# Kernel tuning notes

Measured on AMD Instinct MI355X. Metric: run time of the kernel, lower is better.

Reference implementation:

```python
import jax, jax.numpy as jnp
import numpy as np

EMBED_DIM = 1024
NUM_HEADS = 16
HEAD_DIM = EMBED_DIM // NUM_HEADS
SCALE = HEAD_DIM ** -0.5


def setup_inputs() -> dict:
    key = jax.random.key(0)
    ks = jax.random.split(key, 9)
    B, S, E = 2, 2048, EMBED_DIM
    std = E ** -0.5
    return {
        "x": jax.random.normal(ks[0], (B, S, E), dtype=jnp.float32),
        "Wq": jax.random.normal(ks[1], (E, E), dtype=jnp.float32) * std,
        "bq": jax.random.normal(ks[2], (E,), dtype=jnp.float32) * 0.01,
        "Wk": jax.random.normal(ks[3], (E, E), dtype=jnp.float32) * std,
        "bk": jax.random.normal(ks[4], (E,), dtype=jnp.float32) * 0.01,
        "Wv": jax.random.normal(ks[5], (E, E), dtype=jnp.float32) * std,
        "bv": jax.random.normal(ks[6], (E,), dtype=jnp.float32) * 0.01,
        "Wo": jax.random.normal(ks[7], (E, E), dtype=jnp.float32) * std,
        "bo": jax.random.normal(ks[8], (E,), dtype=jnp.float32) * 0.01,
    }


def reference(x, Wq, bq, Wk, bk, Wv, bv, Wo, bo):
    B, S, E = x.shape
    H, D = NUM_HEADS, HEAD_DIM
    # torch Linear: y = x @ W.T + b
    q = (x @ Wq.T + bq).reshape(B, S, H, D).transpose(0, 2, 1, 3)  # [B,H,S,D]
    k = (x @ Wk.T + bk).reshape(B, S, H, D).transpose(0, 2, 1, 3)
    v = (x @ Wv.T + bv).reshape(B, S, H, D).transpose(0, 2, 1, 3)
    attn = jnp.einsum("bhqd,bhkd->bhqk", q, k) * SCALE  # [B,H,S,S]
    # NOTE: original code softmaxes over dim=1 (the heads axis) — faithful repro.
    attn = jax.nn.softmax(attn.astype(jnp.float32), axis=1).astype(q.dtype)
    out = jnp.einsum("bhqk,bhkd->bhqd", attn, v)  # [B,H,S,D]
    out = out.transpose(0, 2, 1, 3).reshape(B, S, E)
    out = out @ Wo.T + bo
    return out, attn
```

## Files before the change

### kernel.cpp

```cpp
#include <hip/hip_runtime.h>

typedef _Float16 hf2 __attribute__((ext_vector_type(2)));
typedef _Float16 hf4 __attribute__((ext_vector_type(4)));
typedef _Float16 hf8 __attribute__((ext_vector_type(8)));
typedef float    fx4 __attribute__((ext_vector_type(4)));

#define GLD16(gp, lp) __builtin_amdgcn_global_load_lds(                      \
    (const __attribute__((address_space(1))) void*)(gp),                     \
    (__attribute__((address_space(3))) void*)(lp), 16, 0, 0)

__global__ __launch_bounds__(256) void cvt_x_k(const float* __restrict__ s,
                                               _Float16* __restrict__ d) {
  size_t i = (size_t)blockIdx.x * 256 + threadIdx.x;
  float4 v = ((const float4*)s)[i];
  hf4 o = {(_Float16)v.x, (_Float16)v.y, (_Float16)v.z, (_Float16)v.w};
  *(hf4*)(d + 4 * i) = o;
}

__global__ __launch_bounds__(256) void cvt_w_k(const float* __restrict__ s0,
                                               const float* __restrict__ s1,
                                               const float* __restrict__ s2,
                                               const float* __restrict__ s3,
                                               _Float16* __restrict__ d) {
  const float* s = blockIdx.y == 0 ? s0 : blockIdx.y == 1 ? s1 : blockIdx.y == 2 ? s2 : s3;
  size_t i = (size_t)blockIdx.x * 256 + threadIdx.x;
  float4 v = ((const float4*)s)[i];
  hf4 o = {(_Float16)v.x, (_Float16)v.y, (_Float16)v.z, (_Float16)v.w};
  *(hf4*)(d + (size_t)blockIdx.y * 1048576 + 4 * i) = o;
}

__device__ __forceinline__ void gemm_tile(
    const _Float16* __restrict__ A, const _Float16* __restrict__ B,
    const float* __restrict__ bias, _Float16* __restrict__ Ch,
    float* __restrict__ Cf, int m0, int n0, int ldc, int mode)
{
  __shared__ alignas(16) _Float16 Asm[2][128 * 32];
  __shared__ alignas(16) _Float16 Bsm[2][128 * 32];
  const int tid = (int)threadIdx.x;
  const int lane = tid & 63, wv = tid >> 6;
  const int col = lane & 15, g = lane >> 4;

  fx4 acc[2][8];
#pragma unroll
  for (int i = 0; i < 2; ++i)
#pragma unroll
    for (int j = 0; j < 8; ++j) acc[i][j] = fx4{0.f, 0.f, 0.f, 0.f};

  const int cp0 = tid, cp1 = tid + 256;
  const int row0 = cp0 >> 2, row1 = cp1 >> 2;
  const int ch0 = (cp0 & 3) ^ ((row0 >> 1) & 3);
  const int ch1 = (cp1 & 3) ^ ((row1 >> 1) & 3);
  const _Float16* a0 = A + (size_t)(m0 + row0) * 1024 + ch0 * 8;
  const _Float16* a1 = A + (size_t)(m0 + row1) * 1024 + ch1 * 8;
  const _Float16* b0 = B + (size_t)(n0 + row0) * 1024 + ch0 * 8;
  const _Float16* b1 = B + (size_t)(n0 + row1) * 1024 + ch1 * 8;

  int aoff[2], boff[8];
#pragma unroll
  for (int mi = 0; mi < 2; ++mi) {
    int row = wv * 32 + mi * 16 + col;
    aoff[mi] = (row * 4 + (g ^ ((row >> 1) & 3))) * 8;
  }
#pragma unroll
  for (int nj = 0; nj < 8; ++nj) {
    int row = nj * 16 + col;
    boff[nj] = (row * 4 + (g ^ ((row >> 1) & 3))) * 8;
  }

#define STAGE_T(bufi, kt) {                          \
    GLD16(a0 + (kt) * 32, &Asm[bufi][cp0 * 8]);      \
    GLD16(a1 + (kt) * 32, &Asm[bufi][cp1 * 8]);      \
    GLD16(b0 + (kt) * 32, &Bsm[bufi][cp0 * 8]);      \
    GLD16(b1 + (kt) * 32, &Bsm[bufi][cp1 * 8]); }

  STAGE_T(0, 0);
  int buf = 0;
  for (int kt = 0; kt < 32; ++kt) {
    __syncthreads();
    if (kt + 1 < 32) STAGE_T(buf ^ 1, kt + 1);
    hf8 af[2], bf[8];
#pragma unroll
    for (int mi = 0; mi < 2; ++mi) af[mi] = *(const hf8*)&Asm[buf][aoff[mi]];
#pragma unroll
    for (int nj = 0; nj < 8; ++nj) bf[nj] = *(const hf8*)&Bsm[buf][boff[nj]];
#pragma unroll
    for (int mi = 0; mi < 2; ++mi)
#pragma unroll
      for (int nj = 0; nj < 8; ++nj)
        acc[mi][nj] = __builtin_amdgcn_mfma_f32_16x16x32_f16(af[mi], bf[nj], acc[mi][nj], 0, 0, 0);
    buf ^= 1;
  }
#undef STAGE_T

  if (mode == 2) {
#pragma unroll
    for (int nj = 0; nj < 8; ++nj) {
      float bn = bias[n0 + nj * 16 + col];
#pragma unroll
      for (int mi = 0; mi < 2; ++mi)
#pragma unroll
        for (int r = 0; r < 4; ++r)
          Cf[(size_t)(m0 + wv * 32 + mi * 16 + 4 * g + r) * ldc + n0 + nj * 16 + col] =
              acc[mi][nj][r] + bn;
    }
  } else if (mode == 0) {
#pragma unroll
    for (int nj = 0; nj < 8; ++nj) {
      float bn = bias[n0 + nj * 16 + col];
#pragma unroll
      for (int mi = 0; mi < 2; ++mi)
#pragma unroll
        for (int r = 0; r < 4; ++r)
          Ch[(size_t)(m0 + wv * 32 + mi * 16 + 4 * g + r) * ldc + n0 + nj * 16 + col] =
              (_Float16)(acc[mi][nj][r] + bn);
    }
  } else {
#pragma unroll
    for (int mi = 0; mi < 2; ++mi)
#pragma unroll
      for (int r = 0; r < 4; ++r) {
        float bm = bias[m0 + wv * 32 + mi * 16 + 4 * g + r];
#pragma unroll
        for (int nj = 0; nj < 8; ++nj)
          Ch[(size_t)(m0 + wv * 32 + mi * 16 + 4 * g + r) * ldc + n0 + nj * 16 + col] =
              (_Float16)(acc[mi][nj][r] + bm);
      }
  }
}

__global__ __launch_bounds__(256, 3) void qkv_gemm_k(
    const _Float16* __restrict__ xh, const _Float16* __restrict__ Wqh,
    const _Float16* __restrict__ Wkh, const _Float16* __restrict__ Wvh,
    const float* __restrict__ bq, const float* __restrict__ bk,
    const float* __restrict__ bv, _Float16* __restrict__ Qh,
    _Float16* __restrict__ Kh, _Float16* __restrict__ Vt)
{
  int id = (int)blockIdx.x;
  if (id < 512) {
    int t = id & 255;
    const _Float16* Bp = (id < 256) ? Wqh : Wkh;
    const float*    bp = (id < 256) ? bq : bk;
    _Float16*       Cp = (id < 256) ? Qh : Kh;
    gemm_tile(xh, Bp, bp, Cp, nullptr, (t >> 3) * 128, (t & 7) * 128, 1024, 0);
  } else {
    int t = id - 512;
    gemm_tile(Wvh, xh, bv, Vt, nullptr, (t >> 5) * 128, (t & 31) * 128, 4096, 1);
  }
}

__global__ __launch_bounds__(256, 3) void out_gemm_k(
    const _Float16* __restrict__ Oh, const _Float16* __restrict__ Woh,
    const float* __restrict__ bo, float* __restrict__ outp)
{
  int id = (int)blockIdx.x;
  gemm_tile(Oh, Woh, bo, nullptr, outp, (id >> 3) * 128, (id & 7) * 128, 1024, 2);
}

__global__ __launch_bounds__(256) void repack_v_k(const _Float16* __restrict__ Vt,
                                                  _Float16* __restrict__ V2) {
  const int tid = (int)threadIdx.x;
  const int kgi = (int)blockIdx.x;
  const int h = (int)blockIdx.y, b = (int)blockIdx.z;
  const int k0 = kgi * 128;
  __shared__ alignas(16) _Float16 Vl[64 * 128];
#pragma unroll
  for (int i = 0; i < 4; ++i) {
    int s = tid + i * 256;
    int er = s >> 4, c = s & 15;
    GLD16(Vt + (size_t)(h * 64 + er) * 4096 + b * 2048 + k0 + ((c ^ (er & 15)) * 8),
          Vl + s * 8);
  }
  __syncthreads();
  const int lane = tid & 63, dtsub = tid >> 6;
  const int col = lane & 15, g = lane >> 4;
  const int er = dtsub * 16 + col;
  _Float16* out = V2 + ((((size_t)(b * 16 + h) * 128 + (k0 >> 4)) * 4 + dtsub) * 256) + lane * 4;
#pragma unroll
  for (int ks = 0; ks < 8; ++ks) {
    int cl = 2 * ks + (g >> 1);
    int phys = cl ^ col;
    hf4 v = *(const hf4*)&Vl[er * 128 + phys * 8 + (g & 1) * 4];
    *(hf4*)(out + (size_t)ks * 1024) = v;
  }
}

__global__ __launch_bounds__(256, 4) void qk_stats_k(
    const _Float16* __restrict__ Qh, const _Float16* __restrict__ Kh,
    float* __restrict__ C0, float* __restrict__ C1)
{
  const int tid = (int)threadIdx.x;
  const int lane = tid & 63, wv = tid >> 6;
  const int col = lane & 15, g = lane >> 4;
  const int id = (int)blockIdx.x;
  const int xcd = id & 7, j = id >> 3;
  const int b = xcd >> 2, qq = xcd & 3;
  const int kx = j >> 5, qyl = j & 31;
  const int q0 = (qq * 32 + qyl) * 16;
  const int kt0 = kx * 64;

  __shared__ alignas(16) _Float16 Kt[2][4096];
  __shared__ alignas(16) _Float16 Qt[2][1024];

  const _Float16* Kbase = Kh + (size_t)(b * 2048 + kt0) * 1024;
  const _Float16* Qbase = Qh + (size_t)(b * 2048 + q0) * 1024;
  const int kr0 = tid >> 3,         kc0 = tid & 7;
  const int kr1 = (tid + 256) >> 3, kc1 = (tid + 256) & 7;
  const int qr = tid >> 3,          qc = tid & 7;

#define STG1(bufi, h) {                                                       \
    GLD16(Kbase + (size_t)kr0 * 1024 + (h) * 64 + (kc0 ^ (kr0 & 7)) * 8,      \
          &Kt[bufi][tid * 8]);                                                \
    GLD16(Kbase + (size_t)kr1 * 1024 + (h) * 64 + (kc1 ^ (kr1 & 7)) * 8,      \
          &Kt[bufi][(tid + 256) * 8]);                                        \
    if (tid < 128)                                                            \
      GLD16(Qbase + (size_t)qr * 1024 + (h) * 64 + (qc ^ (qr & 7)) * 8,       \
            &Qt[bufi][tid * 8]); }

  fx4 lg[16];
#pragma unroll
  for (int h = 0; h < 16; ++h) lg[h] = fx4{0.f, 0.f, 0.f, 0.f};

  STG1(0, 0);
  int buf = 0;
  const int krow = wv * 16 + col;
#pragma unroll
  for (int h = 0; h < 16; ++h) {
    __syncthreads();
    if (h < 15) STG1(buf ^ 1, h + 1);
    hf8 ka0 = *(const hf8*)&Kt[buf][krow * 64 + ((0 + g) ^ (krow & 7)) * 8];
    hf8 ka1 = *(const hf8*)&Kt[buf][krow * 64 + ((4 + g) ^ (krow & 7)) * 8];
    hf8 qa0 = *(const hf8*)&Qt[buf][col * 64 + ((0 + g) ^ (col & 7)) * 8];
    hf8 qa1 = *(const hf8*)&Qt[buf][col * 64 + ((4 + g) ^ (col & 7)) * 8];
    lg[h] = __builtin_amdgcn_mfma_f32_16x16x32_f16(ka0, qa0, lg[h], 0, 0, 0);
    lg[h] = __builtin_amdgcn_mfma_f32_16x16x32_f16(ka1, qa1, lg[h], 0, 0, 0);
    buf ^= 1;
  }
#undef STG1

  fx4 mx = lg[0];
#pragma unroll
  for (int h = 1; h < 16; ++h)
#pragma unroll
    for (int r = 0; r < 4; ++r) mx[r] = fmaxf(mx[r], lg[h][r]);
  fx4 sm = fx4{0.f, 0.f, 0.f, 0.f};
#pragma unroll
  for (int h = 0; h < 16; ++h)
#pragma unroll
    for (int r = 0; r < 4; ++r) sm[r] += __expf((lg[h][r] - mx[r]) * 0.125f);
  fx4 C;
#pragma unroll
  for (int r = 0; r < 4; ++r) C[r] = mx[r] * 0.125f + __logf(sm[r]);

  float* Cb = b ? C1 : C0;
  const int ktp = kx * 4 + wv;
  const int qt  = qq * 32 + qyl;
  *(fx4*)(Cb + ((size_t)ktp * 128 + qt) * 256 + lane * 4) = C;
}

__global__ __launch_bounds__(512, 4) void pv_attn_k(
    const _Float16* __restrict__ Qh, const _Float16* __restrict__ Kh,
    const _Float16* __restrict__ V2, const float* __restrict__ C0,
    const float* __restrict__ C1, float* __restrict__ attnp,
    _Float16* __restrict__ Oh)
{
  const int tid = (int)threadIdx.x;
  const int lane = tid & 63, wv = tid >> 6;
  const int col = lane & 15, g = lane >> 4;
  const int id = (int)blockIdx.x;
  const int lin = (id & 7) * 256 + (id >> 3);
  const int b = lin >> 10, qt32 = (lin >> 4) & 63, h = lin & 15;
  const int q0 = qt32 * 32;

  __shared__ alignas(16) _Float16 Kt[2][8192];
  __shared__ alignas(16) _Float16 Qt[2048];
  __shared__ alignas(16) float    sst[2][16][136];

  const _Float16* Kbh = Kh + (size_t)(b * 2048) * 1024 + h * 64;
  const float*    Cb  = b ? C1 : C0;

#define STGK2(bufi, kc) {                                                     \
    int r0_ = tid >> 3, c0_ = tid & 7;                                        \
    int r1_ = (tid + 512) >> 3, c1_ = (tid + 512) & 7;                        \
    GLD16(Kbh + (size_t)((kc) * 128 + r0_) * 1024 + (c0_ ^ (r0_ & 7)) * 8,    \
          &Kt[bufi][tid * 8]);                                                \
    GLD16(Kbh + (size_t)((kc) * 128 + r1_) * 1024 + (c1_ ^ (r1_ & 7)) * 8,    \
          &Kt[bufi][(tid + 512) * 8]); }

  if (tid < 256) {
    int qr_ = tid >> 3, qc_ = tid & 7;
    GLD16(Qh + (size_t)(b * 2048 + q0 + qr_) * 1024 + h * 64 + (qc_ ^ (qr_ & 7)) * 8,
          &Qt[tid * 8]);
  }

  fx4 acc[2][4];
#pragma unroll
  for (int t = 0; t < 2; ++t)
#pragma unroll
    for (int dt = 0; dt < 4; ++dt) acc[t][dt] = fx4{0.f, 0.f, 0.f, 0.f};

  STGK2(0, 0);
  int buf = 0;
  const int krow = wv * 16 + col;
  const int srow = 2 * wv + (lane >> 5);
  const int sks  = (lane & 31) * 4;
  float* attnbase = attnp + (size_t)((b * 16 + h) * 2048 + q0) * 2048;
  const _Float16* v2h = V2 + (size_t)(b * 16 + h) * 131072 + lane * 4;

  for (int kc = 0; kc < 16; ++kc) {
    __syncthreads();
    if (kc < 15) STGK2(buf ^ 1, kc + 1);

    hf8 ka0 = *(const hf8*)&Kt[buf][krow * 64 + ((0 + g) ^ (krow & 7)) * 8];
    hf8 ka1 = *(const hf8*)&Kt[buf][krow * 64 + ((4 + g) ^ (krow & 7)) * 8];

    const int ksg = kc * 8 + wv;
    const _Float16* v2b = v2h + (size_t)ksg * 1024;
    hf4 vb[4];
#pragma unroll
    for (int dt = 0; dt < 4; ++dt) vb[dt] = *(const hf4*)(v2b + dt * 256);

#pragma unroll
    for (int t = 0; t < 2; ++t) {
      const int qrow = t * 16 + col;
      hf8 qa0 = *(const hf8*)&Qt[qrow * 64 + ((0 + g) ^ (qrow & 7)) * 8];
      hf8 qa1 = *(const hf8*)&Qt[qrow * 64 + ((4 + g) ^ (qrow & 7)) * 8];
      fx4 lg = fx4{0.f, 0.f, 0.f, 0.f};
      lg = __builtin_amdgcn_mfma_f32_16x16x32_f16(ka0, qa0, lg, 0, 0, 0);
      lg = __builtin_amdgcn_mfma_f32_16x16x32_f16(ka1, qa1, lg, 0, 0, 0);

      fx4 cc = *(const fx4*)(Cb + ((size_t)ksg * 128 + qt32 * 2 + t) * 256 + lane * 4);
      fx4 av;
#pragma unroll
      for (int r = 0; r < 4; ++r) av[r] = __expf(lg[r] * 0.125f - cc[r]);

      hf4 pa = {(_Float16)av[0], (_Float16)av[1], (_Float16)av[2], (_Float16)av[3]};
#pragma unroll
      for (int dt = 0; dt < 4; ++dt)
        acc[t][dt] = __builtin_amdgcn_mfma_f32_16x16x16f16(pa, vb[dt], acc[t][dt], 0, 0, 0);

      *(fx4*)&sst[t][col][wv * 16 + 4 * g] = av;
    }
    __syncthreads();

#pragma unroll
    for (int t = 0; t < 2; ++t) {
      fx4 val = *(const fx4*)&sst[t][srow][sks];
      __builtin_nontemporal_store(
          val, (fx4*)(attnbase + (size_t)(t * 16 + srow) * 2048 + kc * 128 + sks));
    }
    buf ^= 1;
  }
#undef STGK2

  float* Osum = &sst[0][0][0];
  for (int w = 0; w < 8; ++w) {
    __syncthreads();
    if (wv == w) {
#pragma unroll
      for (int t = 0; t < 2; ++t)
#pragma unroll
        for (int dt = 0; dt < 4; ++dt)
#pragma unroll
          for (int r = 0; r < 4; ++r) {
            int idx = (t * 16 + 4 * g + r) * 64 + dt * 16 + col;
            Osum[idx] = (w == 0) ? acc[t][dt][r] : Osum[idx] + acc[t][dt][r];
          }
    }
  }
  __syncthreads();
  {
    int q = tid >> 4, e4 = (tid & 15) * 4;
    hf4 o = {(_Float16)Osum[q * 64 + e4],     (_Float16)Osum[q * 64 + e4 + 1],
             (_Float16)Osum[q * 64 + e4 + 2], (_Float16)Osum[q * 64 + e4 + 3]};
    *(hf4*)(Oh + (size_t)(b * 2048 + q0 + q) * 1024 + h * 64 + e4) = o;
  }
}

extern "C" void kernel_launch(void* const* d_in, const int* in_sizes, int n_in,
                              void* d_out, int out_size, void* d_ws, size_t ws_size,
                              hipStream_t stream) {
  (void)in_sizes; (void)n_in; (void)out_size; (void)ws_size;
  const float* x  = (const float*)d_in[0];
  const float* Wq = (const float*)d_in[1];
  const float* bq = (const float*)d_in[2];
  const float* Wk = (const float*)d_in[3];
  const float* bk = (const float*)d_in[4];
  const float* Wv = (const float*)d_in[5];
  const float* bv = (const float*)d_in[6];
  const float* Wo = (const float*)d_in[7];
  const float* bo = (const float*)d_in[8];

  char* ws = (char*)d_ws;
  _Float16* xh   = (_Float16*)(ws + (0ull  << 20));
  _Float16* V2   = (_Float16*)(ws + (0ull  << 20));
  _Float16* Wqh  = (_Float16*)(ws + (8ull  << 20));
  _Float16* Wkh  = (_Float16*)(ws + (10ull << 20));
  _Float16* Wvh  = (_Float16*)(ws + (12ull << 20));
  _Float16* Woh  = (_Float16*)(ws + (14ull << 20));
  _Float16* Qh   = (_Float16*)(ws + (16ull << 20));
  _Float16* Kh   = (_Float16*)(ws + (24ull << 20));
  _Float16* Vt   = (_Float16*)(ws + (32ull << 20));
  _Float16* Oh   = (_Float16*)(ws + (40ull << 20));
  float*    C1   = (float*)   (ws + (48ull << 20));

  float* outp  = (float*)d_out;
  float* C0    = outp;
  float* attnp = outp + 4194304ull;

  cvt_x_k<<<4096, 256, 0, stream>>>(x, xh);
  cvt_w_k<<<dim3(1024, 4), 256, 0, stream>>>(Wq, Wk, Wv, Wo, Wqh);
  qkv_gemm_k<<<768, 256, 0, stream>>>(xh, Wqh, Wkh, Wvh, bq, bk, bv, Qh, Kh, Vt);
  repack_v_k<<<dim3(16, 16, 2), 256, 0, stream>>>(Vt, V2);
  qk_stats_k<<<8192, 256, 0, stream>>>(Qh, Kh, C0, C1);
  pv_attn_k<<<2048, 512, 0, stream>>>(Qh, Kh, V2, C0, C1, attnp, Oh);
  out_gemm_k<<<256, 256, 0, stream>>>(Oh, Woh, bo, outp);
}
```

Measured before the change: 299.3 us.

## Stage two heads per step in QK stats; double query tile in PV attention

The QK-statistics kernel now loads K and Q tiles covering two heads (128 columns) per pipeline step with a 16-way XOR swizzle. That halves the number of barrier/prefetch iterations. The PV-attention kernel now processes 64 query rows per block instead of 32 and is launched with half as many blocks, so each staged K tile and V fragment is reused across twice as many queries. The trade-off is larger LDS use and more accumulator registers, which may lower occupancy. The Osum reduction buffer must also hold 64x64 floats, which fits within the enlarged sst array.

```diff
diff --git a/kernel.cpp b/kernel.cpp
--- a/kernel.cpp
+++ b/kernel.cpp
@@ -198,23 +198,22 @@
   const int q0 = (qq * 32 + qyl) * 16;
   const int kt0 = kx * 64;
 
-  __shared__ alignas(16) _Float16 Kt[2][4096];
-  __shared__ alignas(16) _Float16 Qt[2][1024];
+  __shared__ alignas(16) _Float16 Kt[2][8192];
+  __shared__ alignas(16) _Float16 Qt[2][2048];
 
   const _Float16* Kbase = Kh + (size_t)(b * 2048 + kt0) * 1024;
   const _Float16* Qbase = Qh + (size_t)(b * 2048 + q0) * 1024;
-  const int kr0 = tid >> 3,         kc0 = tid & 7;
-  const int kr1 = (tid + 256) >> 3, kc1 = (tid + 256) & 7;
-  const int qr = tid >> 3,          qc = tid & 7;
-
-#define STG1(bufi, h) {                                                       \
-    GLD16(Kbase + (size_t)kr0 * 1024 + (h) * 64 + (kc0 ^ (kr0 & 7)) * 8,      \
-          &Kt[bufi][tid * 8]);                                                \
-    GLD16(Kbase + (size_t)kr1 * 1024 + (h) * 64 + (kc1 ^ (kr1 & 7)) * 8,      \
-          &Kt[bufi][(tid + 256) * 8]);                                        \
-    if (tid < 128)                                                            \
-      GLD16(Qbase + (size_t)qr * 1024 + (h) * 64 + (qc ^ (qr & 7)) * 8,       \
-            &Qt[bufi][tid * 8]); }
+
+#define STG1(bufi, hp) {                                                      \
+    _Pragma("unroll")                                                         \
+    for (int i_ = 0; i_ < 4; ++i_) {                                          \
+      int s_ = tid + i_ * 256, r_ = s_ >> 4, pc_ = s_ & 15;                   \
+      GLD16(Kbase + (size_t)r_ * 1024 + (hp) * 128 + ((pc_ ^ (r_ & 15)) * 8), \
+            &Kt[bufi][s_ * 8]);                                               \
+    }                                                                         \
+    { int r_ = tid >> 4, pc_ = tid & 15;                                      \
+      GLD16(Qbase + (size_t)r_ * 1024 + (hp) * 128 + ((pc_ ^ r_) * 8),        \
+            &Qt[bufi][tid * 8]); } }
 
   fx4 lg[16];
 #pragma unroll
@@ -224,15 +223,19 @@
   int buf = 0;
   const int krow = wv * 16 + col;
 #pragma unroll
-  for (int h = 0; h < 16; ++h) {
+  for (int hp = 0; hp < 8; ++hp) {
     __syncthreads();
-    if (h < 15) STG1(buf ^ 1, h + 1);
-    hf8 ka0 = *(const hf8*)&Kt[buf][krow * 64 + ((0 + g) ^ (krow & 7)) * 8];
-    hf8 ka1 = *(const hf8*)&Kt[buf][krow * 64 + ((4 + g) ^ (krow & 7)) * 8];
-    hf8 qa0 = *(const hf8*)&Qt[buf][col * 64 + ((0 + g) ^ (col & 7)) * 8];
-    hf8 qa1 = *(const hf8*)&Qt[buf][col * 64 + ((4 + g) ^ (col & 7)) * 8];
-    lg[h] = __builtin_amdgcn_mfma_f32_16x16x32_f16(ka0, qa0, lg[h], 0, 0, 0);
-    lg[h] = __builtin_amdgcn_mfma_f32_16x16x32_f16(ka1, qa1, lg[h], 0, 0, 0);
+    if (hp < 7) STG1(buf ^ 1, hp + 1);
+#pragma unroll
+    for (int hh = 0; hh < 2; ++hh) {
+      const int h = 2 * hp + hh;
+      hf8 ka0 = *(const hf8*)&Kt[buf][krow * 128 + (((hh * 8 + 0 + g) ^ (krow & 15)) * 8)];
+      hf8 ka1 = *(const hf8*)&Kt[buf][krow * 128 + (((hh * 8 + 4 + g) ^ (krow & 15)) * 8)];
+      hf8 qa0 = *(const hf8*)&Qt[buf][col * 128 + (((hh * 8 + 0 + g) ^ col) * 8)];
+      hf8 qa1 = *(const hf8*)&Qt[buf][col * 128 + (((hh * 8 + 4 + g) ^ col) * 8)];
+      lg[h] = __builtin_amdgcn_mfma_f32_16x16x32_f16(ka0, qa0, lg[h], 0, 0, 0);
+      lg[h] = __builtin_amdgcn_mfma_f32_16x16x32_f16(ka1, qa1, lg[h], 0, 0, 0);
+    }
     buf ^= 1;
   }
 #undef STG1
@@ -267,13 +270,13 @@
   const int lane = tid & 63, wv = tid >> 6;
   const int col = lane & 15, g = lane >> 4;
   const int id = (int)blockIdx.x;
-  const int lin = (id & 7) * 256 + (id >> 3);
-  const int b = lin >> 10, qt32 = (lin >> 4) & 63, h = lin & 15;
-  const int q0 = qt32 * 32;
+  const int lin = (id & 7) * 128 + (id >> 3);
+  const int b = lin >> 9, qt64 = (lin >> 4) & 31, h = lin & 15;
+  const int q0 = qt64 * 64;
 
   __shared__ alignas(16) _Float16 Kt[2][8192];
-  __shared__ alignas(16) _Float16 Qt[2048];
-  __shared__ alignas(16) float    sst[2][16][136];
+  __shared__ alignas(16) _Float16 Qt[4096];
+  __shared__ alignas(16) float    sst[4][16][136];
 
   const _Float16* Kbh = Kh + (size_t)(b * 2048) * 1024 + h * 64;
   const float*    Cb  = b ? C1 : C0;
@@ -286,15 +289,15 @@
     GLD16(Kbh + (size_t)((kc) * 128 + r1_) * 1024 + (c1_ ^ (r1_ & 7)) * 8,    \
           &Kt[bufi][(tid + 512) * 8]); }
 
-  if (tid < 256) {
+  {
     int qr_ = tid >> 3, qc_ = tid & 7;
     GLD16(Qh + (size_t)(b * 2048 + q0 + qr_) * 1024 + h * 64 + (qc_ ^ (qr_ & 7)) * 8,
           &Qt[tid * 8]);
   }
 
-  fx4 acc[2][4];
-#pragma unroll
-  for (int t = 0; t < 2; ++t)
+  fx4 acc[4][4];
+#pragma unroll
+  for (int t = 0; t < 4; ++t)
 #pragma unroll
     for (int dt = 0; dt < 4; ++dt) acc[t][dt] = fx4{0.f, 0.f, 0.f, 0.f};
 
@@ -320,7 +323,7 @@
     for (int dt = 0; dt < 4; ++dt) vb[dt] = *(const hf4*)(v2b + dt * 256);
 
 #pragma unroll
-    for (int t = 0; t < 2; ++t) {
+    for (int t = 0; t < 4; ++t) {
       const int qrow = t * 16 + col;
       hf8 qa0 = *(const hf8*)&Qt[qrow * 64 + ((0 + g) ^ (qrow & 7)) * 8];
       hf8 qa1 = *(const hf8*)&Qt[qrow * 64 + ((4 + g) ^ (qrow & 7)) * 8];
@@ -328,7 +331,7 @@
       lg = __builtin_amdgcn_mfma_f32_16x16x32_f16(ka0, qa0, lg, 0, 0, 0);
       lg = __builtin_amdgcn_mfma_f32_16x16x32_f16(ka1, qa1, lg, 0, 0, 0);
 
-      fx4 cc = *(const fx4*)(Cb + ((size_t)ksg * 128 + qt32 * 2 + t) * 256 + lane * 4);
+      fx4 cc = *(const fx4*)(Cb + ((size_t)ksg * 128 + qt64 * 4 + t) * 256 + lane * 4);
       fx4 av;
 #pragma unroll
       for (int r = 0; r < 4; ++r) av[r] = __expf(lg[r] * 0.125f - cc[r]);
@@ -343,7 +346,7 @@
     __syncthreads();
 
 #pragma unroll
-    for (int t = 0; t < 2; ++t) {
+    for (int t = 0; t < 4; ++t) {
       fx4 val = *(const fx4*)&sst[t][srow][sks];
       __builtin_nontemporal_store(
           val, (fx4*)(attnbase + (size_t)(t * 16 + srow) * 2048 + kc * 128 + sks));
@@ -357,7 +360,7 @@
     __syncthreads();
     if (wv == w) {
 #pragma unroll
-      for (int t = 0; t < 2; ++t)
+      for (int t = 0; t < 4; ++t)
 #pragma unroll
         for (int dt = 0; dt < 4; ++dt)
 #pragma unroll
@@ -368,8 +371,10 @@
     }
   }
   __syncthreads();
-  {
-    int q = tid >> 4, e4 = (tid & 15) * 4;
+#pragma unroll
+  for (int it = 0; it < 2; ++it) {
+    int s = tid + it * 512;
+    int q = s >> 4, e4 = (s & 15) * 4;
     hf4 o = {(_Float16)Osum[q * 64 + e4],     (_Float16)Osum[q * 64 + e4 + 1],
              (_Float16)Osum[q * 64 + e4 + 2], (_Float16)Osum[q * 64 + e4 + 3]};
     *(hf4*)(Oh + (size_t)(b * 2048 + q0 + q) * 1024 + h * 64 + e4) = o;
@@ -412,6 +417,6 @@
   qkv_gemm_k<<<768, 256, 0, stream>>>(xh, Wqh, Wkh, Wvh, bq, bk, bv, Qh, Kh, Vt);
   repack_v_k<<<dim3(16, 16, 2), 256, 0, stream>>>(Vt, V2);
   qk_stats_k<<<8192, 256, 0, stream>>>(Qh, Kh, C0, C1);
-  pv_attn_k<<<2048, 512, 0, stream>>>(Qh, Kh, V2, C0, C1, attnp, Oh);
+  pv_attn_k<<<1024, 512, 0, stream>>>(Qh, Kh, V2, C0, C1, attnp, Oh);
   out_gemm_k<<<256, 256, 0, stream>>>(Oh, Woh, bo, outp);
 }
```

Result: no change. 294.8 us (-1.5%).
